# Kernel tuning notes

Hardware: AMD Instinct MI355X
Metric: run time of the kernel (lower is better)

The kernel has to match this reference:

```python
import jax, jax.numpy as jnp
import numpy as np

N = 4096
DIM_IN = 256
DIM_H = DIM_IN // 2  # 128
DIM_OUT = 128


def setup_inputs() -> dict:
    key = jax.random.key(0)
    ks = jax.random.split(key, 8)
    # Normalized-adjacency-like dense matrices (scaled so propagation is stable
    # and exp() of the score matrix does not overflow).
    A_s = jax.random.uniform(ks[0], (N, N), dtype=jnp.float32) * (1.0 / N)
    A_t = jax.random.uniform(ks[1], (N, N), dtype=jnp.float32) * (1.0 / N)
    X_s = jax.random.normal(ks[2], (N, DIM_IN), dtype=jnp.float32) * 0.1
    X_t = jax.random.normal(ks[3], (N, DIM_IN), dtype=jnp.float32) * 0.1
    # Linear weights (bias=False). Stored as [in, out] for x @ W.
    W1 = jax.random.normal(ks[4], (DIM_IN, DIM_H), dtype=jnp.float32) / np.sqrt(DIM_IN)
    W2 = jax.random.normal(ks[5], (DIM_H, DIM_H), dtype=jnp.float32) / np.sqrt(DIM_H)
    W3 = jax.random.normal(ks[6], (DIM_H, DIM_H), dtype=jnp.float32) / np.sqrt(DIM_H)
    W4 = jax.random.normal(ks[7], (DIM_H, DIM_OUT), dtype=jnp.float32) / np.sqrt(DIM_H)
    return {"A_s": A_s, "X_s": X_s, "A_t": A_t, "X_t": X_t,
            "W1": W1, "W2": W2, "W3": W3, "W4": W4}


def reference(A_s, X_s, A_t, X_t, W1, W2, W3, W4):
    # Two GCN propagation layers per graph: relu((A @ X) @ W)
    Xs = jax.nn.relu((A_s @ X_s) @ W1)   # [N, DIM_H]
    Xs = jax.nn.relu((A_s @ Xs) @ W2)    # [N, DIM_H]
    Xt = jax.nn.relu((A_t @ X_t) @ W1)
    Xt = jax.nn.relu((A_t @ Xt) @ W2)
    # Unnormalized exp cross-attention scores: [N, N]
    S = jnp.exp((Xs @ W3) @ Xt.T)
    out_s = (S @ Xs) @ W4                # [N, DIM_OUT]
    out_t = (S @ Xt) @ W4                # [N, DIM_OUT]
    return (out_s, out_t, S)
```

## Files before the change

kernel.cpp:

```cpp
#include <hip/hip_runtime.h>
#include <stdint.h>

typedef __attribute__((ext_vector_type(4))) float f32x4;
typedef __attribute__((ext_vector_type(8))) short s16x8;

typedef const __attribute__((address_space(1))) void* gas_ptr;
typedef __attribute__((address_space(3))) void* las_ptr;

__device__ __forceinline__ unsigned short f2b(float f) {
    union { float f; unsigned u; } v; v.f = f;
    unsigned r = v.u + 0x7fffu + ((v.u >> 16) & 1u);
    return (unsigned short)(r >> 16);
}

__device__ __forceinline__ unsigned pack2(float f0, float f1) {
    union { float f; unsigned u; } a, b;
    a.f = f0; b.f = f1;
    return __builtin_amdgcn_perm(b.u + 0x8000u, a.u + 0x8000u, 0x07060302u);
}

__global__ void cast2_bf16_k(const float* __restrict__ a, unsigned short* __restrict__ da,
                             const float* __restrict__ b, unsigned short* __restrict__ db,
                             int n4) {
    int i = blockIdx.x * blockDim.x + threadIdx.x;
    int stride = gridDim.x * blockDim.x;
    for (; i < n4; i += stride) {
        float4 va = ((const float4*)a)[i];
        ushort4 pa; pa.x = f2b(va.x); pa.y = f2b(va.y); pa.z = f2b(va.z); pa.w = f2b(va.w);
        ((ushort4*)da)[i] = pa;
        float4 vb = ((const float4*)b)[i];
        ushort4 pb; pb.x = f2b(vb.x); pb.y = f2b(vb.y); pb.z = f2b(vb.z); pb.w = f2b(vb.w);
        ((ushort4*)db)[i] = pb;
    }
}

template<int Z>
__global__ void reduceZ_relu_cast_k(const float* __restrict__ P, unsigned short* __restrict__ d,
                                    int n4, int slice4) {
    int i = blockIdx.x * blockDim.x + threadIdx.x;
    int stride = gridDim.x * blockDim.x;
    for (; i < n4; i += stride) {
        f32x4 s = ((const f32x4*)P)[i];
        #pragma unroll
        for (int z = 1; z < Z; z++) s += ((const f32x4*)P)[i + (size_t)z * slice4];
        ushort4 p;
        p.x = f2b(fmaxf(s[0], 0.f)); p.y = f2b(fmaxf(s[1], 0.f));
        p.z = f2b(fmaxf(s[2], 0.f)); p.w = f2b(fmaxf(s[3], 0.f));
        ((ushort4*)d)[i] = p;
    }
}

template<int Z>
__global__ void reduceZ_fold_k(const float* __restrict__ P, float* __restrict__ out) {
    const int n4 = 4096 * 256 / 4;
    int i = blockIdx.x * blockDim.x + threadIdx.x;
    int stride = gridDim.x * blockDim.x;
    for (; i < n4; i += stride) {
        f32x4 s = ((const f32x4*)P)[i];
        #pragma unroll
        for (int z = 1; z < Z; z++) s += ((const f32x4*)P)[i + (size_t)z * n4];
        const int m = i >> 6;
        const int c = (i & 63) << 2;
        float* o = out + ((c >> 7) ? (size_t)4096 * 128 : 0) + (size_t)m * 128 + (c & 127);
        *(f32x4*)(void*)o = s;
    }
}

__global__ void transpose_w_k(const float* __restrict__ W1, const float* __restrict__ W2,
                              const float* __restrict__ W3, const float* __restrict__ W4,
                              unsigned short* __restrict__ W1t, unsigned short* __restrict__ W2t,
                              unsigned short* __restrict__ W3t, unsigned short* __restrict__ W4t) {
    __shared__ float tile[32][33];
    const float* src; unsigned short* dst; int R, C;
    switch (blockIdx.z) {
        case 0: src = W1; dst = W1t; R = 256; C = 128; break;
        case 1: src = W2; dst = W2t; R = 128; C = 128; break;
        case 2: src = W3; dst = W3t; R = 128; C = 128; break;
        default: src = W4; dst = W4t; R = 128; C = 128; break;
    }
    int c0 = blockIdx.x * 32, r0 = blockIdx.y * 32;
    if (r0 >= R) return;
    int tx = threadIdx.x & 31, ty = threadIdx.x >> 5;
    #pragma unroll
    for (int rr = ty; rr < 32; rr += 8)
        tile[rr][tx] = src[(size_t)(r0 + rr) * C + c0 + tx];
    __syncthreads();
    #pragma unroll
    for (int rr = ty; rr < 32; rr += 8)
        dst[(size_t)(c0 + rr) * R + r0 + tx] = f2b(tile[tx][rr]);
}

enum { EP_BF16 = 0, EP_T = 1, EP_TFOLD = 2, EP_EXP = 3, EP_PART = 4 };

template<int BM, int BN, int FM, int FN, int EPI>
__global__ void __launch_bounds__(256)
gemm_nt(const unsigned short* __restrict__ A, const unsigned short* __restrict__ B,
        int lda, int ldb, int kchunk,
        float* __restrict__ Cf, unsigned short* __restrict__ Cb,
        unsigned short* __restrict__ Ct, int ldc, int ldct)
{
    constexpr int BK = 64;
    constexpr int SEG = BK / 8;
    __shared__ __align__(16) short As[BM * BK];
    __shared__ __align__(16) short Bs[BN * BK];

    const int t = threadIdx.x;
    const int lane = t & 63;
    const int w = t >> 6;
    const int wr = w >> 1, wc = w & 1;
    const int m0 = blockIdx.x * BM;
    const int n0 = blockIdx.y * BN;
    const int k0 = blockIdx.z * kchunk;

    f32x4 acc[FM][FN];
    #pragma unroll
    for (int i = 0; i < FM; i++)
        #pragma unroll
        for (int j = 0; j < FN; j++) acc[i][j] = (f32x4){0.f, 0.f, 0.f, 0.f};

    const int KT = kchunk >> 6;
    const int mrow = lane & 15;
    const int q = lane >> 4;

    for (int kt = 0; kt < KT; ++kt) {
        const int kk = k0 + (kt << 6);
        #pragma unroll
        for (int idx = t; idx < BM * SEG; idx += 256) {
            const int row = idx >> 3, seg = idx & 7;
            const int gseg = seg ^ (row & 7);
            const unsigned short* g = A + (size_t)(m0 + row) * lda + kk + (gseg << 3);
            __builtin_amdgcn_global_load_lds((gas_ptr)g, (las_ptr)(As + idx * 8), 16, 0, 0);
        }
        #pragma unroll
        for (int idx = t; idx < BN * SEG; idx += 256) {
            const int row = idx >> 3, seg = idx & 7;
            const int gseg = seg ^ (row & 7);
            const unsigned short* g = B + (size_t)(n0 + row) * ldb + kk + (gseg << 3);
            __builtin_amdgcn_global_load_lds((gas_ptr)g, (las_ptr)(Bs + idx * 8), 16, 0, 0);
        }
        __syncthreads();

        #pragma unroll
        for (int kq = 0; kq < 2; ++kq) {
            s16x8 af[FM], bfr[FN];
            #pragma unroll
            for (int i = 0; i < FM; i++) {
                const int r = wr * FM * 16 + i * 16 + mrow;
                const int sg = (kq * 4 + q) ^ (r & 7);
                af[i] = *(const s16x8*)(const void*)(As + r * BK + (sg << 3));
            }
            #pragma unroll
            for (int j = 0; j < FN; j++) {
                const int r = wc * FN * 16 + j * 16 + mrow;
                const int sg = (kq * 4 + q) ^ (r & 7);
                bfr[j] = *(const s16x8*)(const void*)(Bs + r * BK + (sg << 3));
            }
            #pragma unroll
            for (int i = 0; i < FM; i++)
                #pragma unroll
                for (int j = 0; j < FN; j++)
                    acc[i][j] = __builtin_amdgcn_mfma_f32_16x16x32_bf16(af[i], bfr[j], acc[i][j], 0, 0, 0);
        }
        __syncthreads();
    }

    const int cn = lane & 15;
    const int q4 = (lane >> 4) << 2;
    #pragma unroll
    for (int i = 0; i < FM; i++) {
        const int mb = m0 + wr * FM * 16 + i * 16 + q4;
        #pragma unroll
        for (int j = 0; j < FN; j++) {
            const int nn = n0 + wc * FN * 16 + j * 16 + cn;
            if constexpr (EPI == EP_BF16) {
                #pragma unroll
                for (int r = 0; r < 4; r++)
                    Cb[(size_t)(mb + r) * ldc + nn] = f2b(acc[i][j][r]);
            } else if constexpr (EPI == EP_T) {
                ushort4 p;
                p.x = f2b(acc[i][j][0]); p.y = f2b(acc[i][j][1]);
                p.z = f2b(acc[i][j][2]); p.w = f2b(acc[i][j][3]);
                *(ushort4*)(void*)(Ct + (size_t)nn * ldct + mb) = p;
            } else if constexpr (EPI == EP_TFOLD) {
                ushort4 p;
                p.x = f2b(acc[i][j][0]); p.y = f2b(acc[i][j][1]);
                p.z = f2b(acc[i][j][2]); p.w = f2b(acc[i][j][3]);
                const int trow = nn + ((mb >> 12) << 7);
                *(ushort4*)(void*)(Ct + (size_t)trow * ldct + (mb & 4095)) = p;
            } else if constexpr (EPI == EP_EXP) {
                #pragma unroll
                for (int r = 0; r < 4; r++) {
                    float v = __expf(acc[i][j][r]);
                    __builtin_nontemporal_store(v, Cf + (size_t)(mb + r) * ldc + nn);
                    Cb[(size_t)(mb + r) * ldc + nn] = f2b(v);
                }
            } else if constexpr (EPI == EP_PART) {
                float* base = Cf + (size_t)blockIdx.z * ((size_t)4096 * 256);
                #pragma unroll
                for (int r = 0; r < 4; r++)
                    base[(size_t)(mb + r) * ldc + nn] = acc[i][j][r];
            }
        }
    }
}

__global__ void __launch_bounds__(256)
pz_fused(const unsigned short* __restrict__ X2,
         const unsigned short* __restrict__ W3t, const unsigned short* __restrict__ W4t,
         unsigned short* __restrict__ Pb, unsigned short* __restrict__ ZcatT)
{
    const bool isP = (blockIdx.y == 1);
    if (isP && blockIdx.x >= 128) return;
    const unsigned short* B = isP ? W3t : W4t;

    __shared__ __align__(16) short As[32 * 32];
    __shared__ __align__(16) short Bs[128 * 32];

    const int t = threadIdx.x;
    const int lane = t & 63;
    const int w = t >> 6;
    const int wr = w >> 1, wc = w & 1;
    const int m0 = blockIdx.x * 32;

    f32x4 acc[4];
    #pragma unroll
    for (int j = 0; j < 4; j++) acc[j] = (f32x4){0.f, 0.f, 0.f, 0.f};

    const int mrow = lane & 15;
    const int q8 = (lane >> 4) << 3;

    for (int kt = 0; kt < 4; ++kt) {
        const int kk = kt << 5;
        if (t < 128) {
            const unsigned short* g = X2 + (size_t)(m0 + (t >> 2)) * 128 + kk + ((t & 3) << 3);
            __builtin_amdgcn_global_load_lds((gas_ptr)g, (las_ptr)(As + t * 8), 16, 0, 0);
        }
        #pragma unroll
        for (int idx = t; idx < 512; idx += 256) {
            const unsigned short* g = B + (size_t)(idx >> 2) * 128 + kk + ((idx & 3) << 3);
            __builtin_amdgcn_global_load_lds((gas_ptr)g, (las_ptr)(Bs + idx * 8), 16, 0, 0);
        }
        __syncthreads();

        s16x8 af = *(const s16x8*)(const void*)(As + (wr * 16 + mrow) * 32 + q8);
        #pragma unroll
        for (int j = 0; j < 4; j++) {
            s16x8 bf = *(const s16x8*)(const void*)(Bs + (wc * 64 + j * 16 + mrow) * 32 + q8);
            acc[j] = __builtin_amdgcn_mfma_f32_16x16x32_bf16(af, bf, acc[j], 0, 0, 0);
        }
        __syncthreads();
    }

    const int cn = lane & 15;
    const int q4 = (lane >> 4) << 2;
    const int mb = m0 + wr * 16 + q4;
    #pragma unroll
    for (int j = 0; j < 4; j++) {
        const int nn = wc * 64 + j * 16 + cn;
        if (isP) {
            #pragma unroll
            for (int r = 0; r < 4; r++)
                Pb[(size_t)(mb + r) * 128 + nn] = f2b(acc[j][r]);
        } else {
            ushort4 p;
            p.x = f2b(acc[j][0]); p.y = f2b(acc[j][1]);
            p.z = f2b(acc[j][2]); p.w = f2b(acc[j][3]);
            const int trow = nn + ((mb >> 12) << 7);
            *(ushort4*)(void*)(ZcatT + (size_t)trow * 4096 + (mb & 4095)) = p;
        }
    }
}

__global__ void __launch_bounds__(256)
gemm_a32_nt(const float* __restrict__ A, const float* __restrict__ A2,
            const unsigned short* __restrict__ B, const unsigned short* __restrict__ B2,
            int Mhalf, int lda, int ldb, int kchunk, float* __restrict__ Cf, int ldc)
{
    __shared__ __align__(16) float As[64 * 64];
    __shared__ __align__(16) short Bs[128 * 64];

    const int t = threadIdx.x;
    const int lane = t & 63;
    const int w = t >> 6;
    const int wr = w >> 1, wc = w & 1;
    const int m0 = blockIdx.x * 64;
    const int n0 = blockIdx.y * 128;
    const int k0 = blockIdx.z * kchunk;

    const float* Ap = A;
    const unsigned short* Bp = B;
    int am0 = m0;
    if (m0 >= Mhalf) { Ap = A2; Bp = B2; am0 = m0 - Mhalf; }

    f32x4 acc[2][4];
    #pragma unroll
    for (int i = 0; i < 2; i++)
        #pragma unroll
        for (int j = 0; j < 4; j++) acc[i][j] = (f32x4){0.f, 0.f, 0.f, 0.f};

    const int KT = kchunk >> 6;
    const int mrow = lane & 15;
    const int q = lane >> 4;

    for (int kt = 0; kt < KT; ++kt) {
        const int kk = k0 + (kt << 6);
        #pragma unroll
        for (int it = 0; it < 4; ++it) {
            int idx = it * 256 + t;
            int row = idx >> 4, seg = idx & 15;
            int gseg = seg ^ (row & 7);
            const float* g = Ap + (size_t)(am0 + row) * lda + kk + (gseg << 2);
            __builtin_amdgcn_global_load_lds((gas_ptr)g, (las_ptr)(As + idx * 4), 16, 0, 0);
        }
        #pragma unroll
        for (int it = 0; it < 4; ++it) {
            int idx = it * 256 + t;
            int row = idx >> 3, seg = idx & 7;
            int gseg = seg ^ (row & 7);
            const unsigned short* g = Bp + (size_t)(n0 + row) * ldb + kk + (gseg << 3);
            __builtin_amdgcn_global_load_lds((gas_ptr)g, (las_ptr)(Bs + idx * 8), 16, 0, 0);
        }
        __syncthreads();

        #pragma unroll
        for (int kq = 0; kq < 2; ++kq) {
            s16x8 af[2], bfr[4];
            #pragma unroll
            for (int i = 0; i < 2; i++) {
                const int r = wr * 32 + i * 16 + mrow;
                const int s0 = (kq * 8 + q * 2) ^ (r & 7);
                const int s1 = (kq * 8 + q * 2 + 1) ^ (r & 7);
                const f32x4 lo = *(const f32x4*)(const void*)(As + r * 64 + (s0 << 2));
                const f32x4 hi = *(const f32x4*)(const void*)(As + r * 64 + (s1 << 2));
                union { s16x8 v; unsigned u[4]; } pk;
                pk.u[0] = pack2(lo[0], lo[1]); pk.u[1] = pack2(lo[2], lo[3]);
                pk.u[2] = pack2(hi[0], hi[1]); pk.u[3] = pack2(hi[2], hi[3]);
                af[i] = pk.v;
            }
            #pragma unroll
            for (int j = 0; j < 4; j++) {
                const int r = wc * 64 + j * 16 + mrow;
                const int sg = (kq * 4 + q) ^ (r & 7);
                bfr[j] = *(const s16x8*)(const void*)(Bs + r * 64 + (sg << 3));
            }
            #pragma unroll
            for (int i = 0; i < 2; i++)
                #pragma unroll
                for (int j = 0; j < 4; j++)
                    acc[i][j] = __builtin_amdgcn_mfma_f32_16x16x32_bf16(af[i], bfr[j], acc[i][j], 0, 0, 0);
        }
        __syncthreads();
    }

    float* base = Cf + (size_t)blockIdx.z * ((size_t)8192 * 128);
    const int cn = lane & 15;
    const int q4 = (lane >> 4) << 2;
    #pragma unroll
    for (int i = 0; i < 2; i++) {
        const int mb = m0 + wr * 32 + i * 16 + q4;
        #pragma unroll
        for (int j = 0; j < 4; j++) {
            const int nn = n0 + wc * 64 + j * 16 + cn;
            #pragma unroll
            for (int r = 0; r < 4; r++)
                base[(size_t)(mb + r) * ldc + nn] = acc[i][j][r];
        }
    }
}

extern "C" void kernel_launch(void* const* d_in, const int* in_sizes, int n_in,
                              void* d_out, int out_size, void* d_ws, size_t ws_size,
                              hipStream_t stream) {
    const int N = 4096;
    const float* A_s = (const float*)d_in[0];
    const float* X_s = (const float*)d_in[1];
    const float* A_t = (const float*)d_in[2];
    const float* X_t = (const float*)d_in[3];
    const float* W1  = (const float*)d_in[4];
    const float* W2  = (const float*)d_in[5];
    const float* W3  = (const float*)d_in[6];
    const float* W4  = (const float*)d_in[7];

    float* out   = (float*)d_out;
    float* S_out = out + (size_t)2 * N * 128;

    char* ws = (char*)d_ws;
    unsigned short* Xcatb = (unsigned short*)(ws + 0);
    unsigned short* W1t   = (unsigned short*)(ws + 4194304);
    unsigned short* W2t   = (unsigned short*)(ws + 4259840);
    unsigned short* W3t   = (unsigned short*)(ws + 4292608);
    unsigned short* W4t   = (unsigned short*)(ws + 4325376);
    unsigned short* Y1T   = (unsigned short*)(ws + 4718592);
    unsigned short* X1b   = (unsigned short*)(ws + 6815744);
    unsigned short* X2b   = (unsigned short*)(ws + 8912896);
    unsigned short* Pb    = (unsigned short*)(ws + 11010048);
    unsigned short* ZcatT = (unsigned short*)(ws + 12058624);
    float*          Pf    = (float*)(ws + 14155776);
    unsigned short* Sb    = (unsigned short*)(ws + 47710208);
    unsigned short* Xt2b  = X2b + (size_t)N * 128;

    cast2_bf16_k<<<512, 256, 0, stream>>>(X_s, Xcatb, X_t, Xcatb + (size_t)N * 256, N * 256 / 4);
    transpose_w_k<<<dim3(4, 8, 4), 256, 0, stream>>>(W1, W2, W3, W4, W1t, W2t, W3t, W4t);

    gemm_nt<32, 128, 1, 4, EP_T><<<dim3(256, 1, 1), 256, 0, stream>>>(
        Xcatb, W1t, 256, 256, 256, nullptr, nullptr, Y1T, 0, 8192);

    gemm_a32_nt<<<dim3(128, 1, 4), 256, 0, stream>>>(
        A_s, A_t, Y1T, Y1T + 4096, 4096, 4096, 8192, 1024, Pf, 128);
    reduceZ_relu_cast_k<4><<<1024, 256, 0, stream>>>(Pf, X1b, 8192 * 128 / 4, 8192 * 128 / 4);

    gemm_nt<32, 128, 1, 4, EP_T><<<dim3(256, 1, 1), 256, 0, stream>>>(
        X1b, W2t, 128, 128, 128, nullptr, nullptr, Y1T, 0, 8192);

    gemm_a32_nt<<<dim3(128, 1, 4), 256, 0, stream>>>(
        A_s, A_t, Y1T, Y1T + 4096, 4096, 4096, 8192, 1024, Pf, 128);
    reduceZ_relu_cast_k<4><<<1024, 256, 0, stream>>>(Pf, X2b, 8192 * 128 / 4, 8192 * 128 / 4);

    pz_fused<<<dim3(256, 2, 1), 256, 0, stream>>>(X2b, W3t, W4t, Pb, ZcatT);

    gemm_nt<128, 128, 4, 4, EP_EXP><<<dim3(32, 32, 1), 256, 0, stream>>>(
        Pb, Xt2b, 128, 128, 128, S_out, Sb, nullptr, 4096, 0);

    gemm_nt<64, 128, 2, 4, EP_PART><<<dim3(64, 2, 4), 256, 0, stream>>>(
        Sb, ZcatT, 4096, 4096, 1024, Pf, nullptr, nullptr, 256, 0);
    reduceZ_fold_k<4><<<1024, 256, 0, stream>>>(Pf, out);
}
```

Baseline: 291.6 us.

## Double-buffer LDS loads in the A-propagation and S@Z GEMMs

Converts the fp32-A propagation GEMM to a two-stage LDS pipeline. The next K-tile's global_load_lds is issued before computing on the current tile, and explicit vmcnt waits plus raw barriers replace __syncthreads. A new dedicated bf16 double-buffered kernel replaces the generic gemm_nt for the S@Zcat split-K GEMM. The aim is to hide global memory latency behind MFMA work, at the cost of doubling LDS use, which may lower occupancy. The hand-set waitcnt values carry a correctness risk if they do not match the number of outstanding loads.

```diff
diff --git a/kernel.cpp b/kernel.cpp
--- a/kernel.cpp
+++ b/kernel.cpp
@@ -6,6 +6,10 @@
 
 typedef const __attribute__((address_space(1))) void* gas_ptr;
 typedef __attribute__((address_space(3))) void* las_ptr;
+
+#define WAIT_VM8 (8 | 0x70 | 0xF00)
+#define WAIT_VM6 (6 | 0x70 | 0xF00)
+#define WAIT_VM0 (0 | 0x70 | 0xF00)
 
 __device__ __forceinline__ unsigned short f2b(float f) {
     union { float f; unsigned u; } v; v.f = f;
@@ -181,12 +185,6 @@
                 p.x = f2b(acc[i][j][0]); p.y = f2b(acc[i][j][1]);
                 p.z = f2b(acc[i][j][2]); p.w = f2b(acc[i][j][3]);
                 *(ushort4*)(void*)(Ct + (size_t)nn * ldct + mb) = p;
-            } else if constexpr (EPI == EP_TFOLD) {
-                ushort4 p;
-                p.x = f2b(acc[i][j][0]); p.y = f2b(acc[i][j][1]);
-                p.z = f2b(acc[i][j][2]); p.w = f2b(acc[i][j][3]);
-                const int trow = nn + ((mb >> 12) << 7);
-                *(ushort4*)(void*)(Ct + (size_t)trow * ldct + (mb & 4095)) = p;
             } else if constexpr (EPI == EP_EXP) {
                 #pragma unroll
                 for (int r = 0; r < 4; r++) {
@@ -272,12 +270,12 @@
 }
 
 __global__ void __launch_bounds__(256)
-gemm_a32_nt(const float* __restrict__ A, const float* __restrict__ A2,
-            const unsigned short* __restrict__ B, const unsigned short* __restrict__ B2,
-            int Mhalf, int lda, int ldb, int kchunk, float* __restrict__ Cf, int ldc)
+gemm_a32_pipe(const float* __restrict__ A, const float* __restrict__ A2,
+              const unsigned short* __restrict__ B, const unsigned short* __restrict__ B2,
+              int Mhalf, int lda, int ldb, int kchunk, float* __restrict__ Cf, int ldc)
 {
-    __shared__ __align__(16) float As[64 * 64];
-    __shared__ __align__(16) short Bs[128 * 64];
+    __shared__ __align__(16) float Asf[2][64 * 64];
+    __shared__ __align__(16) short Bsb[2][128 * 64];
 
     const int t = threadIdx.x;
     const int lane = t & 63;
@@ -302,7 +300,7 @@
     const int mrow = lane & 15;
     const int q = lane >> 4;
 
-    for (int kt = 0; kt < KT; ++kt) {
+    auto stage = [&](int kt, int p) {
         const int kk = k0 + (kt << 6);
         #pragma unroll
         for (int it = 0; it < 4; ++it) {
@@ -310,7 +308,7 @@
             int row = idx >> 4, seg = idx & 15;
             int gseg = seg ^ (row & 7);
             const float* g = Ap + (size_t)(am0 + row) * lda + kk + (gseg << 2);
-            __builtin_amdgcn_global_load_lds((gas_ptr)g, (las_ptr)(As + idx * 4), 16, 0, 0);
+            __builtin_amdgcn_global_load_lds((gas_ptr)g, (las_ptr)(&Asf[p][idx * 4]), 16, 0, 0);
         }
         #pragma unroll
         for (int it = 0; it < 4; ++it) {
@@ -318,9 +316,20 @@
             int row = idx >> 3, seg = idx & 7;
             int gseg = seg ^ (row & 7);
             const unsigned short* g = Bp + (size_t)(n0 + row) * ldb + kk + (gseg << 3);
-            __builtin_amdgcn_global_load_lds((gas_ptr)g, (las_ptr)(Bs + idx * 8), 16, 0, 0);
-        }
-        __syncthreads();
+            __builtin_amdgcn_global_load_lds((gas_ptr)g, (las_ptr)(&Bsb[p][idx * 8]), 16, 0, 0);
+        }
+    };
+
+    stage(0, 0);
+    for (int kt = 0; kt < KT; ++kt) {
+        const int p = kt & 1;
+        if (kt + 1 < KT) {
+            stage(kt + 1, p ^ 1);
+            __builtin_amdgcn_s_waitcnt(WAIT_VM8);
+        } else {
+            __builtin_amdgcn_s_waitcnt(WAIT_VM0);
+        }
+        __builtin_amdgcn_s_barrier();
 
         #pragma unroll
         for (int kq = 0; kq < 2; ++kq) {
@@ -330,8 +339,8 @@
                 const int r = wr * 32 + i * 16 + mrow;
                 const int s0 = (kq * 8 + q * 2) ^ (r & 7);
                 const int s1 = (kq * 8 + q * 2 + 1) ^ (r & 7);
-                const f32x4 lo = *(const f32x4*)(const void*)(As + r * 64 + (s0 << 2));
-                const f32x4 hi = *(const f32x4*)(const void*)(As + r * 64 + (s1 << 2));
+                const f32x4 lo = *(const f32x4*)(const void*)(&Asf[p][r * 64 + (s0 << 2)]);
+                const f32x4 hi = *(const f32x4*)(const void*)(&Asf[p][r * 64 + (s1 << 2)]);
                 union { s16x8 v; unsigned u[4]; } pk;
                 pk.u[0] = pack2(lo[0], lo[1]); pk.u[1] = pack2(lo[2], lo[3]);
                 pk.u[2] = pack2(hi[0], hi[1]); pk.u[3] = pack2(hi[2], hi[3]);
@@ -341,7 +350,7 @@
             for (int j = 0; j < 4; j++) {
                 const int r = wc * 64 + j * 16 + mrow;
                 const int sg = (kq * 4 + q) ^ (r & 7);
-                bfr[j] = *(const s16x8*)(const void*)(Bs + r * 64 + (sg << 3));
+                bfr[j] = *(const s16x8*)(const void*)(&Bsb[p][r * 64 + (sg << 3)]);
             }
             #pragma unroll
             for (int i = 0; i < 2; i++)
@@ -349,10 +358,106 @@
                 for (int j = 0; j < 4; j++)
                     acc[i][j] = __builtin_amdgcn_mfma_f32_16x16x32_bf16(af[i], bfr[j], acc[i][j], 0, 0, 0);
         }
-        __syncthreads();
+        __builtin_amdgcn_s_barrier();
     }
 
     float* base = Cf + (size_t)blockIdx.z * ((size_t)8192 * 128);
+    const int cn = lane & 15;
+    const int q4 = (lane >> 4) << 2;
+    #pragma unroll
+    for (int i = 0; i < 2; i++) {
+        const int mb = m0 + wr * 32 + i * 16 + q4;
+        #pragma unroll
+        for (int j = 0; j < 4; j++) {
+            const int nn = n0 + wc * 64 + j * 16 + cn;
+            #pragma unroll
+            for (int r = 0; r < 4; r++)
+                base[(size_t)(mb + r) * ldc + nn] = acc[i][j][r];
+        }
+    }
+}
+
+__global__ void __launch_bounds__(256)
+gemm_sz_pipe(const unsigned short* __restrict__ A, const unsigned short* __restrict__ B,
+             int lda, int ldb, int kchunk, float* __restrict__ Cf, int ldc)
+{
+    __shared__ __align__(16) short Asb[2][64 * 64];
+    __shared__ __align__(16) short Bsb[2][128 * 64];
+
+    const int t = threadIdx.x;
+    const int lane = t & 63;
+    const int w = t >> 6;
+    const int wr = w >> 1, wc = w & 1;
+    const int m0 = blockIdx.x * 64;
+    const int n0 = blockIdx.y * 128;
+    const int k0 = blockIdx.z * kchunk;
+
+    f32x4 acc[2][4];
+    #pragma unroll
+    for (int i = 0; i < 2; i++)
+        #pragma unroll
+        for (int j = 0; j < 4; j++) acc[i][j] = (f32x4){0.f, 0.f, 0.f, 0.f};
+
+    const int KT = kchunk >> 6;
+    const int mrow = lane & 15;
+    const int q = lane >> 4;
+
+    auto stage = [&](int kt, int p) {
+        const int kk = k0 + (kt << 6);
+        #pragma unroll
+        for (int it = 0; it < 2; ++it) {
+            int idx = it * 256 + t;
+            int row = idx >> 3, seg = idx & 7;
+            int gseg = seg ^ (row & 7);
+            const unsigned short* g = A + (size_t)(m0 + row) * lda + kk + (gseg << 3);
+            __builtin_amdgcn_global_load_lds((gas_ptr)g, (las_ptr)(&Asb[p][idx * 8]), 16, 0, 0);
+        }
+        #pragma unroll
+        for (int it = 0; it < 4; ++it) {
+            int idx = it * 256 + t;
+            int row = idx >> 3, seg = idx & 7;
+            int gseg = seg ^ (row & 7);
+            const unsigned short* g = B + (size_t)(n0 + row) * ldb + kk + (gseg << 3);
+            __builtin_amdgcn_global_load_lds((gas_ptr)g, (las_ptr)(&Bsb[p][idx * 8]), 16, 0, 0);
+        }
+    };
+
+    stage(0, 0);
+    for (int kt = 0; kt < KT; ++kt) {
+        const int p = kt & 1;
+        if (kt + 1 < KT) {
+            stage(kt + 1, p ^ 1);
+            __builtin_amdgcn_s_waitcnt(WAIT_VM6);
+        } else {
+            __builtin_amdgcn_s_waitcnt(WAIT_VM0);
+        }
+        __builtin_amdgcn_s_barrier();
+
+        #pragma unroll
+        for (int kq = 0; kq < 2; ++kq) {
+            s16x8 af[2], bfr[4];
+            #pragma unroll
+            for (int i = 0; i < 2; i++) {
+                const int r = wr * 32 + i * 16 + mrow;
+                const int sg = (kq * 4 + q) ^ (r & 7);
+                af[i] = *(const s16x8*)(const void*)(&Asb[p][r * 64 + (sg << 3)]);
+            }
+            #pragma unroll
+            for (int j = 0; j < 4; j++) {
+                const int r = wc * 64 + j * 16 + mrow;
+                const int sg = (kq * 4 + q) ^ (r & 7);
+                bfr[j] = *(const s16x8*)(const void*)(&Bsb[p][r * 64 + (sg << 3)]);
+            }
+            #pragma unroll
+            for (int i = 0; i < 2; i++)
+                #pragma unroll
+                for (int j = 0; j < 4; j++)
+                    acc[i][j] = __builtin_amdgcn_mfma_f32_16x16x32_bf16(af[i], bfr[j], acc[i][j], 0, 0, 0);
+        }
+        __builtin_amdgcn_s_barrier();
+    }
+
+    float* base = Cf + (size_t)blockIdx.z * ((size_t)4096 * 256);
     const int cn = lane & 15;
     const int q4 = (lane >> 4) << 2;
     #pragma unroll
@@ -405,14 +510,14 @@
     gemm_nt<32, 128, 1, 4, EP_T><<<dim3(256, 1, 1), 256, 0, stream>>>(
         Xcatb, W1t, 256, 256, 256, nullptr, nullptr, Y1T, 0, 8192);
 
-    gemm_a32_nt<<<dim3(128, 1, 4), 256, 0, stream>>>(
+    gemm_a32_pipe<<<dim3(128, 1, 4), 256, 0, stream>>>(
         A_s, A_t, Y1T, Y1T + 4096, 4096, 4096, 8192, 1024, Pf, 128);
     reduceZ_relu_cast_k<4><<<1024, 256, 0, stream>>>(Pf, X1b, 8192 * 128 / 4, 8192 * 128 / 4);
 
     gemm_nt<32, 128, 1, 4, EP_T><<<dim3(256, 1, 1), 256, 0, stream>>>(
         X1b, W2t, 128, 128, 128, nullptr, nullptr, Y1T, 0, 8192);
 
-    gemm_a32_nt<<<dim3(128, 1, 4), 256, 0, stream>>>(
+    gemm_a32_pipe<<<dim3(128, 1, 4), 256, 0, stream>>>(
         A_s, A_t, Y1T, Y1T + 4096, 4096, 4096, 8192, 1024, Pf, 128);
     reduceZ_relu_cast_k<4><<<1024, 256, 0, stream>>>(Pf, X2b, 8192 * 128 / 4, 8192 * 128 / 4);
 
@@ -421,7 +526,7 @@
     gemm_nt<128, 128, 4, 4, EP_EXP><<<dim3(32, 32, 1), 256, 0, stream>>>(
         Pb, Xt2b, 128, 128, 128, S_out, Sb, nullptr, 4096, 0);
 
-    gemm_nt<64, 128, 2, 4, EP_PART><<<dim3(64, 2, 4), 256, 0, stream>>>(
-        Sb, ZcatT, 4096, 4096, 1024, Pf, nullptr, nullptr, 256, 0);
+    gemm_sz_pipe<<<dim3(64, 2, 4), 256, 0, stream>>>(
+        Sb, ZcatT, 4096, 4096, 1024, Pf, 256);
     reduceZ_fold_k<4><<<1024, 256, 0, stream>>>(Pf, out);
 }
```

Result: no change. 289.9 us (-0.6%).
